# Performance work log

Measured on AMD Instinct MI355X. Metric: run time of the kernel, lower is better.

Reference implementation:

```python
import jax, jax.numpy as jnp
import numpy as np

NUM_EXPERTS = 32
INPUT_DIM = 1024
OUTPUT_DIM = 1024  # must equal INPUT_DIM for the original broadcast to work
BATCH = 8192


def setup_inputs() -> dict:
    key = jax.random.key(0)
    k_x, k_w, k_gw, k_gb = jax.random.split(key, 4)
    x = jax.random.normal(k_x, (BATCH, INPUT_DIM), dtype=jnp.float32)
    experts_weights = jax.random.normal(k_w, (NUM_EXPERTS, INPUT_DIM, OUTPUT_DIM), dtype=jnp.float32)
    experts_bias = jnp.zeros((NUM_EXPERTS, OUTPUT_DIM), dtype=jnp.float32)
    # gating Linear(input_dim, num_experts)
    bound = 1.0 / np.sqrt(INPUT_DIM)
    gate_weight = jax.random.uniform(k_gw, (NUM_EXPERTS, INPUT_DIM), minval=-bound, maxval=bound, dtype=jnp.float32)
    gate_bias = jax.random.uniform(k_gb, (NUM_EXPERTS,), minval=-bound, maxval=bound, dtype=jnp.float32)
    return {
        "x": x,
        "experts_weights": experts_weights,
        "experts_bias": experts_bias,
        "gate_weight": gate_weight,
        "gate_bias": gate_bias,
        "topk": 2,
    }


def reference(x, experts_weights, experts_bias, gate_weight, gate_bias, topk):
    # gating: softmax(Linear(x))  -> [B, E]
    gate_logits = x @ gate_weight.T + gate_bias
    gate_outputs = jax.nn.softmax(gate_logits, axis=-1)
    top_k_values, top_k_indices = jax.lax.top_k(gate_outputs, topk)  # [B,K]
    # Faithful to torch.einsum('bi,eio->bei', x, W): sums over o, yields [B,E,I]
    # = x[b,i] * sum_o W[e,i,o]; then bias [E,O] broadcasts (requires I == O).
    w_sum = experts_weights.sum(axis=2)  # [E, I]
    expert_outputs = x[:, None, :] * w_sum[None, :, :] + experts_bias[None, :, :]  # [B,E,I]
    # gather top-k experts per token: [B,K,I]
    selected = jnp.take_along_axis(expert_outputs, top_k_indices[:, :, None], axis=1)
    output = (selected * top_k_values[:, :, None]).sum(axis=1)  # [B,I]
    return output
```

## Files before the change

kernel.cpp:

```cpp
#include <hip/hip_runtime.h>
#include <math.h>

#define NE 32
#define DIM 1024
#define NB 8192
#define F4ROW (DIM / 4)

#define GATE_BLOCKS 512
#define WSUM_BLOCKS ((NE * DIM) / 4)

__global__ __launch_bounds__(256) void stage1_kernel(
    const float* __restrict__ W,
    const float* __restrict__ x,
    const float* __restrict__ gw,
    const float* __restrict__ gb,
    float* __restrict__ wsum,
    float* __restrict__ topv,
    int*   __restrict__ tope)
{
    const int wave = threadIdx.x >> 6;
    const int lane = threadIdx.x & 63;

    if (blockIdx.x >= GATE_BLOCKS) {
        const int r = (blockIdx.x - GATE_BLOCKS) * 4 + wave;
        const float4* row = (const float4*)(W + (size_t)r * DIM);
        float4 a = row[lane], b = row[lane + 64], c = row[lane + 128], d = row[lane + 192];
        float s = ((a.x + a.y) + (a.z + a.w)) + ((b.x + b.y) + (b.z + b.w)) +
                  ((c.x + c.y) + (c.z + c.w)) + ((d.x + d.y) + (d.z + d.w));
#pragma unroll
        for (int off = 32; off >= 1; off >>= 1) s += __shfl_xor(s, off, 64);
        if (lane == 0) wsum[r] = s;
        return;
    }

    __shared__ float logits[16][NE];
    const int tbase = blockIdx.x * 16 + wave * 4;

    const float4* x4 = (const float4*)x;
    float4 xq[4][4];
#pragma unroll
    for (int tk = 0; tk < 4; ++tk)
#pragma unroll
        for (int j = 0; j < 4; ++j)
            xq[tk][j] = x4[(size_t)(tbase + tk) * F4ROW + lane + 64 * j];

    const float4* gw4 = (const float4*)gw;
#pragma unroll 4
    for (int e = 0; e < NE; ++e) {
        const float4 g0 = gw4[(size_t)e * F4ROW + lane];
        const float4 g1 = gw4[(size_t)e * F4ROW + lane + 64];
        const float4 g2 = gw4[(size_t)e * F4ROW + lane + 128];
        const float4 g3 = gw4[(size_t)e * F4ROW + lane + 192];

        float acc[4];
#pragma unroll
        for (int tk = 0; tk < 4; ++tk) {
            float a = 0.f;
            a = fmaf(xq[tk][0].x, g0.x, a); a = fmaf(xq[tk][0].y, g0.y, a);
            a = fmaf(xq[tk][0].z, g0.z, a); a = fmaf(xq[tk][0].w, g0.w, a);
            a = fmaf(xq[tk][1].x, g1.x, a); a = fmaf(xq[tk][1].y, g1.y, a);
            a = fmaf(xq[tk][1].z, g1.z, a); a = fmaf(xq[tk][1].w, g1.w, a);
            a = fmaf(xq[tk][2].x, g2.x, a); a = fmaf(xq[tk][2].y, g2.y, a);
            a = fmaf(xq[tk][2].z, g2.z, a); a = fmaf(xq[tk][2].w, g2.w, a);
            a = fmaf(xq[tk][3].x, g3.x, a); a = fmaf(xq[tk][3].y, g3.y, a);
            a = fmaf(xq[tk][3].z, g3.z, a); a = fmaf(xq[tk][3].w, g3.w, a);
            acc[tk] = a;
        }
#pragma unroll
        for (int off = 32; off >= 1; off >>= 1) {
            acc[0] += __shfl_xor(acc[0], off, 64);
            acc[1] += __shfl_xor(acc[1], off, 64);
            acc[2] += __shfl_xor(acc[2], off, 64);
            acc[3] += __shfl_xor(acc[3], off, 64);
        }
        if (lane == 0) {
            const float gbe = gb[e];
            logits[wave * 4 + 0][e] = acc[0] + gbe;
            logits[wave * 4 + 1][e] = acc[1] + gbe;
            logits[wave * 4 + 2][e] = acc[2] + gbe;
            logits[wave * 4 + 3][e] = acc[3] + gbe;
        }
    }
    __syncthreads();

    if (lane < 4) {
        const int tok = tbase + lane;
        const float* L = logits[wave * 4 + lane];

        float m = L[0];
#pragma unroll
        for (int e = 1; e < NE; ++e) m = fmaxf(m, L[e]);
        float denom = 0.f;
#pragma unroll
        for (int e = 0; e < NE; ++e) denom += expf(L[e] - m);

        int e0 = 0; float l0 = L[0];
#pragma unroll
        for (int e = 1; e < NE; ++e)
            if (L[e] > l0) { l0 = L[e]; e0 = e; }
        int e1 = -1; float l1 = -INFINITY;
#pragma unroll
        for (int e = 0; e < NE; ++e)
            if (e != e0 && L[e] > l1) { l1 = L[e]; e1 = e; }

        const float inv = 1.0f / denom;
        topv[tok * 2 + 0] = expf(l0 - m) * inv;
        topv[tok * 2 + 1] = expf(l1 - m) * inv;
        tope[tok * 2 + 0] = e0;
        tope[tok * 2 + 1] = e1;
    }
}

__global__ __launch_bounds__(256) void combine_kernel(
    const float* __restrict__ x,
    const float* __restrict__ wsum,
    const float* __restrict__ bias,
    const float* __restrict__ topv,
    const int*   __restrict__ tope,
    float* __restrict__ out)
{
    const int wave = threadIdx.x >> 6;
    const int lane = threadIdx.x & 63;
    const int tok  = blockIdx.x * 4 + wave;

    const float v0 = topv[tok * 2 + 0];
    const float v1 = topv[tok * 2 + 1];
    const int   e0 = tope[tok * 2 + 0];
    const int   e1 = tope[tok * 2 + 1];

    const float4* x4 = (const float4*)(x    + (size_t)tok * DIM);
    const float4* w0 = (const float4*)(wsum + (size_t)e0  * DIM);
    const float4* w1 = (const float4*)(wsum + (size_t)e1  * DIM);
    const float4* b0 = (const float4*)(bias + (size_t)e0  * DIM);
    const float4* b1 = (const float4*)(bias + (size_t)e1  * DIM);
    float4*       o4 = (float4*)(out + (size_t)tok * DIM);

#pragma unroll
    for (int j = 0; j < 4; ++j) {
        const int idx = lane + 64 * j;
        const float4 xv = x4[idx];
        const float4 a0 = w0[idx], a1 = w1[idx];
        const float4 c0 = b0[idx], c1 = b1[idx];
        float4 o;
        o.x = fmaf(v0, fmaf(xv.x, a0.x, c0.x), v1 * fmaf(xv.x, a1.x, c1.x));
        o.y = fmaf(v0, fmaf(xv.y, a0.y, c0.y), v1 * fmaf(xv.y, a1.y, c1.y));
        o.z = fmaf(v0, fmaf(xv.z, a0.z, c0.z), v1 * fmaf(xv.z, a1.z, c1.z));
        o.w = fmaf(v0, fmaf(xv.w, a0.w, c0.w), v1 * fmaf(xv.w, a1.w, c1.w));
        o4[idx] = o;
    }
}

extern "C" void kernel_launch(void* const* d_in, const int* in_sizes, int n_in,
                              void* d_out, int out_size, void* d_ws, size_t ws_size,
                              hipStream_t stream) {
    const float* x    = (const float*)d_in[0];
    const float* W    = (const float*)d_in[1];
    const float* bias = (const float*)d_in[2];
    const float* gw   = (const float*)d_in[3];
    const float* gb   = (const float*)d_in[4];

    float* wsum = (float*)d_ws;
    float* topv = wsum + (size_t)NE * DIM;
    int*   tope = (int*)(topv + (size_t)NB * 2);
    float* out  = (float*)d_out;

    stage1_kernel<<<GATE_BLOCKS + WSUM_BLOCKS, 256, 0, stream>>>(
        W, x, gw, gb, wsum, topv, tope);

    combine_kernel<<<NB / 4, 256, 0, stream>>>(x, wsum, bias, topv, tope, out);
}
```

Before: 57.84 us.

## Fuse gating softmax/top-2 into combine kernel and split wsum into own kernel

Moves the gating matmul, softmax and top-2 selection into the combine kernel, so each wave keeps its two tokens' x rows in registers and reuses them for the output. This removes the second read of x and the topv/tope round trip through memory. The expert weight row-sum becomes a standalone kernel that processes four rows per wave. Top-2 is now done with wave shuffles instead of shared memory, and the gate reuse per wave drops from four tokens to two.

```diff
diff --git a/kernel.cpp b/kernel.cpp
--- a/kernel.cpp
+++ b/kernel.cpp
@@ -4,46 +4,70 @@
 #define NE 32
 #define DIM 1024
 #define NB 8192
-#define F4ROW (DIM / 4)
+#define F4ROW 256
 
-#define GATE_BLOCKS 512
-#define WSUM_BLOCKS ((NE * DIM) / 4)
+__global__ __launch_bounds__(256) void wsum_kernel(const float* __restrict__ W,
+                                                   float* __restrict__ wsum) {
+    const int lane = threadIdx.x & 63;
+    const int wid  = (blockIdx.x * blockDim.x + threadIdx.x) >> 6;
+    const int r0   = wid * 4;
 
-__global__ __launch_bounds__(256) void stage1_kernel(
-    const float* __restrict__ W,
+    const float4* W4 = (const float4*)W;
+    float4 v[4][4];
+#pragma unroll
+    for (int rr = 0; rr < 4; ++rr)
+#pragma unroll
+        for (int j = 0; j < 4; ++j)
+            v[rr][j] = W4[(size_t)(r0 + rr) * F4ROW + lane + 64 * j];
+
+    float s[4];
+#pragma unroll
+    for (int rr = 0; rr < 4; ++rr) {
+        const float4 a = v[rr][0], b = v[rr][1], c = v[rr][2], d = v[rr][3];
+        s[rr] = ((a.x + a.y) + (a.z + a.w)) + ((b.x + b.y) + (b.z + b.w)) +
+                ((c.x + c.y) + (c.z + c.w)) + ((d.x + d.y) + (d.z + d.w));
+    }
+#pragma unroll
+    for (int off = 32; off >= 1; off >>= 1) {
+        s[0] += __shfl_xor(s[0], off, 64);
+        s[1] += __shfl_xor(s[1], off, 64);
+        s[2] += __shfl_xor(s[2], off, 64);
+        s[3] += __shfl_xor(s[3], off, 64);
+    }
+    if (lane == 0) {
+        wsum[r0 + 0] = s[0];
+        wsum[r0 + 1] = s[1];
+        wsum[r0 + 2] = s[2];
+        wsum[r0 + 3] = s[3];
+    }
+}
+
+#define DOT4(acc, xv, gv)                                                      \
+    acc = fmaf((xv).x, (gv).x, acc); acc = fmaf((xv).y, (gv).y, acc);          \
+    acc = fmaf((xv).z, (gv).z, acc); acc = fmaf((xv).w, (gv).w, acc);
+
+__global__ __launch_bounds__(256) void gate_combine_kernel(
     const float* __restrict__ x,
     const float* __restrict__ gw,
     const float* __restrict__ gb,
-    float* __restrict__ wsum,
-    float* __restrict__ topv,
-    int*   __restrict__ tope)
+    const float* __restrict__ wsum,
+    const float* __restrict__ bias,
+    float* __restrict__ out)
 {
+    const int lane = threadIdx.x & 63;
     const int wave = threadIdx.x >> 6;
-    const int lane = threadIdx.x & 63;
+    const int wid  = blockIdx.x * 4 + wave;
+    const int t0   = wid * 2;
 
-    if (blockIdx.x >= GATE_BLOCKS) {
-        const int r = (blockIdx.x - GATE_BLOCKS) * 4 + wave;
-        const float4* row = (const float4*)(W + (size_t)r * DIM);
-        float4 a = row[lane], b = row[lane + 64], c = row[lane + 128], d = row[lane + 192];
-        float s = ((a.x + a.y) + (a.z + a.w)) + ((b.x + b.y) + (b.z + b.w)) +
-                  ((c.x + c.y) + (c.z + c.w)) + ((d.x + d.y) + (d.z + d.w));
+    const float4* x4 = (const float4*)x;
+    float4 xq0[4], xq1[4];
 #pragma unroll
-        for (int off = 32; off >= 1; off >>= 1) s += __shfl_xor(s, off, 64);
-        if (lane == 0) wsum[r] = s;
-        return;
+    for (int j = 0; j < 4; ++j) {
+        xq0[j] = x4[(size_t)(t0 + 0) * F4ROW + lane + 64 * j];
+        xq1[j] = x4[(size_t)(t0 + 1) * F4ROW + lane + 64 * j];
     }
 
-    __shared__ float logits[16][NE];
-    const int tbase = blockIdx.x * 16 + wave * 4;
-
-    const float4* x4 = (const float4*)x;
-    float4 xq[4][4];
-#pragma unroll
-    for (int tk = 0; tk < 4; ++tk)
-#pragma unroll
-        for (int j = 0; j < 4; ++j)
-            xq[tk][j] = x4[(size_t)(tbase + tk) * F4ROW + lane + 64 * j];
-
+    float ml0 = 0.f, ml1 = 0.f;
     const float4* gw4 = (const float4*)gw;
 #pragma unroll 4
     for (int e = 0; e < NE; ++e) {
@@ -52,101 +76,100 @@
         const float4 g2 = gw4[(size_t)e * F4ROW + lane + 128];
         const float4 g3 = gw4[(size_t)e * F4ROW + lane + 192];
 
-        float acc[4];
-#pragma unroll
-        for (int tk = 0; tk < 4; ++tk) {
-            float a = 0.f;
-            a = fmaf(xq[tk][0].x, g0.x, a); a = fmaf(xq[tk][0].y, g0.y, a);
-            a = fmaf(xq[tk][0].z, g0.z, a); a = fmaf(xq[tk][0].w, g0.w, a);
-            a = fmaf(xq[tk][1].x, g1.x, a); a = fmaf(xq[tk][1].y, g1.y, a);
-            a = fmaf(xq[tk][1].z, g1.z, a); a = fmaf(xq[tk][1].w, g1.w, a);
-            a = fmaf(xq[tk][2].x, g2.x, a); a = fmaf(xq[tk][2].y, g2.y, a);
-            a = fmaf(xq[tk][2].z, g2.z, a); a = fmaf(xq[tk][2].w, g2.w, a);
-            a = fmaf(xq[tk][3].x, g3.x, a); a = fmaf(xq[tk][3].y, g3.y, a);
-            a = fmaf(xq[tk][3].z, g3.z, a); a = fmaf(xq[tk][3].w, g3.w, a);
-            acc[tk] = a;
-        }
+        float a0 = 0.f, a1 = 0.f;
+        DOT4(a0, xq0[0], g0); DOT4(a0, xq0[1], g1);
+        DOT4(a0, xq0[2], g2); DOT4(a0, xq0[3], g3);
+        DOT4(a1, xq1[0], g0); DOT4(a1, xq1[1], g1);
+        DOT4(a1, xq1[2], g2); DOT4(a1, xq1[3], g3);
 #pragma unroll
         for (int off = 32; off >= 1; off >>= 1) {
-            acc[0] += __shfl_xor(acc[0], off, 64);
-            acc[1] += __shfl_xor(acc[1], off, 64);
-            acc[2] += __shfl_xor(acc[2], off, 64);
-            acc[3] += __shfl_xor(acc[3], off, 64);
+            a0 += __shfl_xor(a0, off, 64);
+            a1 += __shfl_xor(a1, off, 64);
         }
-        if (lane == 0) {
-            const float gbe = gb[e];
-            logits[wave * 4 + 0][e] = acc[0] + gbe;
-            logits[wave * 4 + 1][e] = acc[1] + gbe;
-            logits[wave * 4 + 2][e] = acc[2] + gbe;
-            logits[wave * 4 + 3][e] = acc[3] + gbe;
+        if (lane == e) { ml0 = a0; ml1 = a1; }
+    }
+    const float gbl = gb[lane & 31];
+    ml0 += gbl;
+    ml1 += gbl;
+
+    auto top2 = [&](float ml, float& ov0, float& ov1, int& oe0, int& oe1) {
+        float m = ml;
+#pragma unroll
+        for (int off = 16; off >= 1; off >>= 1)
+            m = fmaxf(m, __shfl_xor(m, off, 64));
+        float den = expf(ml - m);
+#pragma unroll
+        for (int off = 16; off >= 1; off >>= 1)
+            den += __shfl_xor(den, off, 64);
+        float v = ml; int ix = lane;
+#pragma unroll
+        for (int off = 16; off >= 1; off >>= 1) {
+            const float ovv = __shfl_xor(v, off, 64);
+            const int   oii = __shfl_xor(ix, off, 64);
+            if (ovv > v || (ovv == v && oii < ix)) { v = ovv; ix = oii; }
+        }
+        const int e0 = ix; const float l0 = v;
+        float v2 = (lane == e0) ? -INFINITY : ml; int ix2 = lane;
+#pragma unroll
+        for (int off = 16; off >= 1; off >>= 1) {
+            const float ovv = __shfl_xor(v2, off, 64);
+            const int   oii = __shfl_xor(ix2, off, 64);
+            if (ovv > v2 || (ovv == v2 && oii < ix2)) { v2 = ovv; ix2 = oii; }
+        }
+        const float inv = 1.0f / den;
+        ov0 = expf(l0 - m) * inv;
+        ov1 = expf(v2 - m) * inv;
+        oe0 = e0; oe1 = ix2;
+    };
+
+    float av0, av1; int ae0, ae1;
+    top2(ml0, av0, av1, ae0, ae1);
+    av0 = __shfl(av0, 0, 64); av1 = __shfl(av1, 0, 64);
+    ae0 = __shfl(ae0, 0, 64); ae1 = __shfl(ae1, 0, 64);
+
+    float bv0, bv1; int be0, be1;
+    top2(ml1, bv0, bv1, be0, be1);
+    bv0 = __shfl(bv0, 0, 64); bv1 = __shfl(bv1, 0, 64);
+    be0 = __shfl(be0, 0, 64); be1 = __shfl(be1, 0, 64);
+
+    float4* o4 = (float4*)out;
+    {
+        const float4* w0 = (const float4*)(wsum + (size_t)ae0 * DIM);
+        const float4* w1 = (const float4*)(wsum + (size_t)ae1 * DIM);
+        const float4* c0 = (const float4*)(bias + (size_t)ae0 * DIM);
+        const float4* c1 = (const float4*)(bias + (size_t)ae1 * DIM);
+#pragma unroll
+        for (int j = 0; j < 4; ++j) {
+            const int idx = lane + 64 * j;
+            const float4 xv = xq0[j];
+            const float4 A0 = w0[idx], A1 = w1[idx];
+            const float4 C0 = c0[idx], C1 = c1[idx];
+            float4 o;
+            o.x = fmaf(av0, fmaf(xv.x, A0.x, C0.x), av1 * fmaf(xv.x, A1.x, C1.x));
+            o.y = fmaf(av0, fmaf(xv.y, A0.y, C0.y), av1 * fmaf(xv.y, A1.y, C1.y));
+            o.z = fmaf(av0, fmaf(xv.z, A0.z, C0.z), av1 * fmaf(xv.z, A1.z, C1.z));
+            o.w = fmaf(av0, fmaf(xv.w, A0.w, C0.w), av1 * fmaf(xv.w, A1.w, C1.w));
+            o4[(size_t)(t0 + 0) * F4ROW + idx] = o;
         }
     }
-    __syncthreads();
-
-    if (lane < 4) {
-        const int tok = tbase + lane;
-        const float* L = logits[wave * 4 + lane];
-
-        float m = L[0];
+    {
+        const float4* w0 = (const float4*)(wsum + (size_t)be0 * DIM);
+        const float4* w1 = (const float4*)(wsum + (size_t)be1 * DIM);
+        const float4* c0 = (const float4*)(bias + (size_t)be0 * DIM);
+        const float4* c1 = (const float4*)(bias + (size_t)be1 * DIM);
 #pragma unroll
-        for (int e = 1; e < NE; ++e) m = fmaxf(m, L[e]);
-        float denom = 0.f;
-#pragma unroll
-        for (int e = 0; e < NE; ++e) denom += expf(L[e] - m);
-
-        int e0 = 0; float l0 = L[0];
-#pragma unroll
-        for (int e = 1; e < NE; ++e)
-            if (L[e] > l0) { l0 = L[e]; e0 = e; }
-        int e1 = -1; float l1 = -INFINITY;
-#pragma unroll
-        for (int e = 0; e < NE; ++e)
-            if (e != e0 && L[e] > l1) { l1 = L[e]; e1 = e; }
-
-        const float inv = 1.0f / denom;
-        topv[tok * 2 + 0] = expf(l0 - m) * inv;
-        topv[tok * 2 + 1] = expf(l1 - m) * inv;
-        tope[tok * 2 + 0] = e0;
-        tope[tok * 2 + 1] = e1;
-    }
-}
-
-__global__ __launch_bounds__(256) void combine_kernel(
-    const float* __restrict__ x,
-    const float* __restrict__ wsum,
-    const float* __restrict__ bias,
-    const float* __restrict__ topv,
-    const int*   __restrict__ tope,
-    float* __restrict__ out)
-{
-    const int wave = threadIdx.x >> 6;
-    const int lane = threadIdx.x & 63;
-    const int tok  = blockIdx.x * 4 + wave;
-
-    const float v0 = topv[tok * 2 + 0];
-    const float v1 = topv[tok * 2 + 1];
-    const int   e0 = tope[tok * 2 + 0];
-    const int   e1 = tope[tok * 2 + 1];
-
-    const float4* x4 = (const float4*)(x    + (size_t)tok * DIM);
-    const float4* w0 = (const float4*)(wsum + (size_t)e0  * DIM);
-    const float4* w1 = (const float4*)(wsum + (size_t)e1  * DIM);
-    const float4* b0 = (const float4*)(bias + (size_t)e0  * DIM);
-    const float4* b1 = (const float4*)(bias + (size_t)e1  * DIM);
-    float4*       o4 = (float4*)(out + (size_t)tok * DIM);
-
-#pragma unroll
-    for (int j = 0; j < 4; ++j) {
-        const int idx = lane + 64 * j;
-        const float4 xv = x4[idx];
-        const float4 a0 = w0[idx], a1 = w1[idx];
-        const float4 c0 = b0[idx], c1 = b1[idx];
-        float4 o;
-        o.x = fmaf(v0, fmaf(xv.x, a0.x, c0.x), v1 * fmaf(xv.x, a1.x, c1.x));
-        o.y = fmaf(v0, fmaf(xv.y, a0.y, c0.y), v1 * fmaf(xv.y, a1.y, c1.y));
-        o.z = fmaf(v0, fmaf(xv.z, a0.z, c0.z), v1 * fmaf(xv.z, a1.z, c1.z));
-        o.w = fmaf(v0, fmaf(xv.w, a0.w, c0.w), v1 * fmaf(xv.w, a1.w, c1.w));
-        o4[idx] = o;
+        for (int j = 0; j < 4; ++j) {
+            const int idx = lane + 64 * j;
+            const float4 xv = xq1[j];
+            const float4 A0 = w0[idx], A1 = w1[idx];
+            const float4 C0 = c0[idx], C1 = c1[idx];
+            float4 o;
+            o.x = fmaf(bv0, fmaf(xv.x, A0.x, C0.x), bv1 * fmaf(xv.x, A1.x, C1.x));
+            o.y = fmaf(bv0, fmaf(xv.y, A0.y, C0.y), bv1 * fmaf(xv.y, A1.y, C1.y));
+            o.z = fmaf(bv0, fmaf(xv.z, A0.z, C0.z), bv1 * fmaf(xv.z, A1.z, C1.z));
+            o.w = fmaf(bv0, fmaf(xv.w, A0.w, C0.w), bv1 * fmaf(xv.w, A1.w, C1.w));
+            o4[(size_t)(t0 + 1) * F4ROW + idx] = o;
+        }
     }
 }
 
@@ -160,12 +183,9 @@
     const float* gb   = (const float*)d_in[4];
 
     float* wsum = (float*)d_ws;
-    float* topv = wsum + (size_t)NE * DIM;
-    int*   tope = (int*)(topv + (size_t)NB * 2);
     float* out  = (float*)d_out;
 
-    stage1_kernel<<<GATE_BLOCKS + WSUM_BLOCKS, 256, 0, stream>>>(
-        W, x, gw, gb, wsum, topv, tope);
+    wsum_kernel<<<2048, 256, 0, stream>>>(W, wsum);
 
-    combine_kernel<<<NB / 4, 256, 0, stream>>>(x, wsum, bias, topv, tope, out);
+    gate_combine_kernel<<<1024, 256, 0, stream>>>(x, gw, gb, wsum, bias, out);
 }
```

Measured after the change: 65.78 us. +13.7%, slower.
